# Optimization experiments

Measured on AMD Instinct MI355X. Metric: run time of the kernel, lower is better.

Reference implementation:

```python
import jax, jax.numpy as jnp
import numpy as np

NEG_SLOPE = 0.01   # F.leaky_relu default
EPS_NORM = 1e-12   # F.normalize default eps

N_NODES = 20000
N_RAND_EDGES = 320000
D_IN = 128
D_EMB = 128
C1 = 256
C2 = 32


def _segment_mean(vals, idx, n):
    s = jax.ops.segment_sum(vals, idx, num_segments=n)
    cnt = jax.ops.segment_sum(jnp.ones((vals.shape[0],), vals.dtype), idx, num_segments=n)
    return s / jnp.maximum(cnt, 1.0)[:, None]


def gcn_mean_sparse(h, W, b, src, dst, n):
    # GCN_layer with att=False: copy_u + mean over in-neighbors
    z = h @ W + b
    return _segment_mean(z[src], dst, n)


def gat_sparse(h, W, b, aW, ab, src, dst, n):
    # GCN_layer with att=True on an edge-list graph.
    # att_linear(cat(src,dst)) decomposed: e = leaky_relu(z_src@aWs + z_dst@aWd + ab)
    z = h @ W + b                       # [n, c]
    c = z.shape[-1]
    a_src = (z @ aW[:c])[:, 0]          # [n]
    a_dst = (z @ aW[c:])[:, 0]          # [n]
    e = jax.nn.leaky_relu(a_src[src] + a_dst[dst] + ab[0], NEG_SLOPE)  # [E]
    m = jax.ops.segment_max(e, dst, num_segments=n)                    # softmax over mailbox (per dst)
    alpha = jnp.exp(e - m[dst])
    denom = jax.ops.segment_sum(alpha, dst, num_segments=n)
    num = jax.ops.segment_sum(alpha[:, None] * z[src], dst, num_segments=n)  # [n, c]
    return num / denom[:, None]


def gat_dense(h, W, b, aW, ab):
    # att=True on a complete graph (coarse levels): dense softmax over src axis per dst
    z = h @ W + b                       # [n, c]
    c = z.shape[-1]
    a_src = z @ aW[:c]                  # [n, 1]
    a_dst = z @ aW[c:]                  # [n, 1]
    e = jax.nn.leaky_relu(a_src + a_dst.T + ab[0], NEG_SLOPE)  # [n_src, n_dst]
    alpha = jax.nn.softmax(e, axis=0)
    return jnp.einsum('ij,ic->jc', alpha, z)


def setup_inputs() -> dict:
    key = jax.random.key(0)
    ks = jax.random.split(key, 16)
    feature = jax.random.normal(ks[0], (N_NODES, D_IN), dtype=jnp.float32)
    src = jax.random.randint(ks[1], (N_RAND_EDGES,), 0, N_NODES, dtype=jnp.int32)
    dst = jax.random.randint(ks[2], (N_RAND_EDGES,), 0, N_NODES, dtype=jnp.int32)
    loop = jnp.arange(N_NODES, dtype=jnp.int32)
    edge_index = jnp.stack([jnp.concatenate([src, loop]), jnp.concatenate([dst, loop])])

    def lin(k, fan_in, fan_out):
        s = 1.0 / np.sqrt(fan_in)
        kw, kb = jax.random.split(k)
        W = jax.random.uniform(kw, (fan_in, fan_out), jnp.float32, -s, s)
        b = jax.random.uniform(kb, (fan_out,), jnp.float32, -s, s)
        return W, b

    Wf, bf = lin(ks[3], D_IN, D_EMB)          # GCN_f1
    We1, be1 = lin(ks[4], D_EMB, D_EMB)       # assign layer 1: GCN_emb
    Wa1, ba1 = lin(ks[5], D_EMB, C1)          # assign layer 1: GCN_ass linear
    attW1, attb1 = lin(ks[6], 2 * C1, 1)      # assign layer 1: att_linear
    We2, be2 = lin(ks[7], D_EMB, D_EMB)       # assign layer 2: GCN_emb
    Wa2, ba2 = lin(ks[8], D_EMB, C2)          # assign layer 2: GCN_ass linear
    attW2, attb2 = lin(ks[9], 2 * C2, 1)      # assign layer 2: att_linear
    return dict(feature=feature, edge_index=edge_index,
                Wf=Wf, bf=bf, We1=We1, be1=be1, Wa1=Wa1, ba1=ba1,
                attW1=attW1, attb1=attb1, We2=We2, be2=be2, Wa2=Wa2,
                ba2=ba2, attW2=attW2, attb2=attb2)


def reference(feature, edge_index, Wf, bf, We1, be1, Wa1, ba1, attW1, attb1,
              We2, be2, Wa2, ba2, attW2, attb2):
    src, dst = edge_index[0], edge_index[1]
    n = feature.shape[0]
    # GCN_f1 (att=False) + L2 normalize
    x = gcn_mean_sparse(feature, Wf, bf, src, dst, n)
    x = x / jnp.maximum(jnp.linalg.norm(x, axis=-1, keepdims=True), EPS_NORM)
    embed3 = x                                           # tree_node_embed[3]
    # Assign layer 1 (on original sparse graph)
    z1 = gcn_mean_sparse(x, We1, be1, src, dst, n)       # GCN_emb
    s1 = jax.nn.softmax(gat_sparse(z1, Wa1, ba1, attW1, attb1, src, dst, n), axis=-1)
    x1 = s1.T @ z1                                       # tree_node_embed[2], [C1, D]
    # Coarse graph: s^T A s with strictly positive softmax s -> complete graph
    # (setdiag(0) then add_self_loop => all pairs incl. self loops)
    # Assign layer 2 (dense complete graph over C1 nodes)
    lin2 = x1 @ We2 + be2
    z2 = jnp.broadcast_to(jnp.mean(lin2, axis=0, keepdims=True), lin2.shape)  # mean over all in-neighbors
    s2 = jax.nn.softmax(gat_dense(z2, Wa2, ba2, attW2, attb2), axis=-1)
    x2 = s2.T @ z2                                       # tree_node_embed[1], [C2, D]
    embed0 = jnp.mean(x2)                                # tree_node_embed[0] (scalar mean of all elems)
    assign1 = jnp.ones((s2.shape[-1], 1), dtype=x2.dtype)  # assignmatrix[1]
    # (assignmatrix[3], assignmatrix[2], assignmatrix[1], embed[3], embed[2], embed[1], embed[0])
    return (s1, s2, assign1, embed3, x1, x2, embed0)
```

## Files before the change

kernel.cpp:

```cpp
#include <hip/hip_runtime.h>
#include <hip/hip_bf16.h>
#include <math.h>

#define NN 20000
#define DD 128
#define CC1 256
#define CC2 32
#define X1_SPLIT 128

__global__ void k_count(const int* __restrict__ dst, int* __restrict__ cnt, int E) {
    int e = blockIdx.x * blockDim.x + threadIdx.x;
    if (e < E) atomicAdd(&cnt[dst[e]], 1);
}

__global__ void k_scan(const int* __restrict__ cnt, int* __restrict__ offs, int n) {
    __shared__ int part[1024];
    int t = threadIdx.x;
    int chunk = (n + 1023) / 1024;
    int lo = t * chunk, hi = min(lo + chunk, n);
    int s = 0;
    for (int i = lo; i < hi; i++) s += cnt[i];
    part[t] = s;
    __syncthreads();
    for (int d = 1; d < 1024; d <<= 1) {
        int v = (t >= d) ? part[t - d] : 0;
        __syncthreads();
        part[t] += v;
        __syncthreads();
    }
    int base = (t > 0) ? part[t - 1] : 0;
    for (int i = lo; i < hi; i++) { offs[i] = base; base += cnt[i]; }
    if (t == 1023) offs[n] = part[1023];
}

__global__ void k_fill(const int* __restrict__ src, const int* __restrict__ dst,
                       const int* __restrict__ offs, int* __restrict__ fill,
                       int* __restrict__ csr_src, int E) {
    int e = blockIdx.x * blockDim.x + threadIdx.x;
    if (e < E) {
        int d = dst[e];
        int pos = atomicAdd(&fill[d], 1);
        csr_src[offs[d] + pos] = src[e];
    }
}

__global__ void k_fold(const float* __restrict__ Wa1, const float* __restrict__ ba1,
                       const float* __restrict__ attW1, const float* __restrict__ attb1,
                       float* __restrict__ fold) {
    int t = threadIdx.x;
    float vs = 0.f, vd = 0.f;
    for (int k = 0; k < CC1; k++) {
        float w = Wa1[t * CC1 + k];
        vs += w * attW1[k];
        vd += w * attW1[CC1 + k];
    }
    fold[t] = vs;
    fold[128 + t] = vd;
    if (t == 0) {
        float c = attb1[0];
        for (int k = 0; k < CC1; k++) c += ba1[k] * (attW1[k] + attW1[CC1 + k]);
        fold[256] = c;
    }
}

__global__ __launch_bounds__(256) void k_seg_mean(const float* __restrict__ in,
                                                  const int* __restrict__ offs,
                                                  const int* __restrict__ csr_src,
                                                  float* __restrict__ out, int n) {
    int wave = (blockIdx.x * blockDim.x + threadIdx.x) >> 6;
    int lane = threadIdx.x & 63;
    if (wave >= n) return;
    int lo = offs[wave], hi = offs[wave + 1];
    int half = lane >> 5, l32 = lane & 31;
    const float4* f4 = (const float4*)in;
    float4 acc = make_float4(0.f, 0.f, 0.f, 0.f);
    for (int i = lo + half; i < hi; i += 2) {
        int s = csr_src[i];
        float4 v = f4[(size_t)s * 32 + l32];
        acc.x += v.x; acc.y += v.y; acc.z += v.z; acc.w += v.w;
    }
    acc.x += __shfl_xor(acc.x, 32);
    acc.y += __shfl_xor(acc.y, 32);
    acc.z += __shfl_xor(acc.z, 32);
    acc.w += __shfl_xor(acc.w, 32);
    if (half == 0) {
        float inv = 1.0f / (float)max(hi - lo, 1);
        float4 r = make_float4(acc.x * inv, acc.y * inv, acc.z * inv, acc.w * inv);
        ((float4*)out)[(size_t)wave * 32 + l32] = r;
    }
}

template <int MODE>
__global__ __launch_bounds__(256) void k_gemm128(const float* __restrict__ in,
                                                 const float* __restrict__ W,
                                                 const float* __restrict__ b,
                                                 float* __restrict__ out,
                                                 const float* __restrict__ fold,
                                                 float* __restrict__ a_src,
                                                 float* __restrict__ a_dst,
                                                 int n, int rows_per_block) {
    __shared__ float sW[128 * 128];
    __shared__ float sT[128][32];
    int t = threadIdx.x;
    for (int i = t; i < 128 * 128; i += 256) sW[i] = W[i];
    int lane = t & 63;
    int wv = t >> 6;
    int j4 = (lane & 31) * 4;
    int rh = lane >> 5;
    int rg = wv * 2 + rh;
    float bj0 = b[j4], bj1 = b[j4 + 1], bj2 = b[j4 + 2], bj3 = b[j4 + 3];
    float vs0 = 0.f, vs1 = 0.f, vs2 = 0.f, vs3 = 0.f;
    float vd0 = 0.f, vd1 = 0.f, vd2 = 0.f, vd3 = 0.f;
    if (MODE == 1) {
        vs0 = fold[j4]; vs1 = fold[j4 + 1]; vs2 = fold[j4 + 2]; vs3 = fold[j4 + 3];
        vd0 = fold[128 + j4]; vd1 = fold[128 + j4 + 1]; vd2 = fold[128 + j4 + 2]; vd3 = fold[128 + j4 + 3];
    }
    int row0 = blockIdx.x * rows_per_block;
    int row_end = min(row0 + rows_per_block, n);
    for (int r = row0; r < row_end; r += 32) {
        int nr = min(32, row_end - r);
        __syncthreads();
        {
            int lrow = t >> 3, seg = t & 7;
            if (lrow < nr) {
                const float4* g = (const float4*)&in[(size_t)(r + lrow) * 128 + seg * 16];
                float4 v0 = g[0], v1 = g[1], v2 = g[2], v3 = g[3];
                int k0 = seg * 16;
                sT[k0 + 0][lrow] = v0.x; sT[k0 + 1][lrow] = v0.y; sT[k0 + 2][lrow] = v0.z; sT[k0 + 3][lrow] = v0.w;
                sT[k0 + 4][lrow] = v1.x; sT[k0 + 5][lrow] = v1.y; sT[k0 + 6][lrow] = v1.z; sT[k0 + 7][lrow] = v1.w;
                sT[k0 + 8][lrow] = v2.x; sT[k0 + 9][lrow] = v2.y; sT[k0 + 10][lrow] = v2.z; sT[k0 + 11][lrow] = v2.w;
                sT[k0 + 12][lrow] = v3.x; sT[k0 + 13][lrow] = v3.y; sT[k0 + 14][lrow] = v3.z; sT[k0 + 15][lrow] = v3.w;
            }
        }
        __syncthreads();
        float acc[4][4];
        #pragma unroll
        for (int p = 0; p < 4; p++) { acc[p][0] = bj0; acc[p][1] = bj1; acc[p][2] = bj2; acc[p][3] = bj3; }
        for (int k = 0; k < 128; k++) {
            float4 w4 = *(const float4*)&sW[k * 128 + j4];
            float4 rv = *(const float4*)&sT[k][rg * 4];
            acc[0][0] += rv.x * w4.x; acc[0][1] += rv.x * w4.y; acc[0][2] += rv.x * w4.z; acc[0][3] += rv.x * w4.w;
            acc[1][0] += rv.y * w4.x; acc[1][1] += rv.y * w4.y; acc[1][2] += rv.y * w4.z; acc[1][3] += rv.y * w4.w;
            acc[2][0] += rv.z * w4.x; acc[2][1] += rv.z * w4.y; acc[2][2] += rv.z * w4.z; acc[2][3] += rv.z * w4.w;
            acc[3][0] += rv.w * w4.x; acc[3][1] += rv.w * w4.y; acc[3][2] += rv.w * w4.z; acc[3][3] += rv.w * w4.w;
        }
        #pragma unroll
        for (int p = 0; p < 4; p++) {
            int row = r + rg * 4 + p;
            if (MODE == 0) {
                float ss_ = acc[p][0] * acc[p][0] + acc[p][1] * acc[p][1] +
                            acc[p][2] * acc[p][2] + acc[p][3] * acc[p][3];
                ss_ += __shfl_xor(ss_, 16); ss_ += __shfl_xor(ss_, 8);
                ss_ += __shfl_xor(ss_, 4);  ss_ += __shfl_xor(ss_, 2); ss_ += __shfl_xor(ss_, 1);
                if (row < row_end) {
                    float scale = 1.0f / fmaxf(sqrtf(ss_), 1e-12f);
                    float4 o = make_float4(acc[p][0] * scale, acc[p][1] * scale, acc[p][2] * scale, acc[p][3] * scale);
                    *(float4*)&out[(size_t)row * 128 + j4] = o;
                }
            } else {
                if (row < row_end) {
                    float4 o = make_float4(acc[p][0], acc[p][1], acc[p][2], acc[p][3]);
                    *(float4*)&out[(size_t)row * 128 + j4] = o;
                }
                float ps = acc[p][0] * vs0 + acc[p][1] * vs1 + acc[p][2] * vs2 + acc[p][3] * vs3;
                float pd = acc[p][0] * vd0 + acc[p][1] * vd1 + acc[p][2] * vd2 + acc[p][3] * vd3;
                ps += __shfl_xor(ps, 16); ps += __shfl_xor(ps, 8); ps += __shfl_xor(ps, 4);
                ps += __shfl_xor(ps, 2);  ps += __shfl_xor(ps, 1);
                pd += __shfl_xor(pd, 16); pd += __shfl_xor(pd, 8); pd += __shfl_xor(pd, 4);
                pd += __shfl_xor(pd, 2);  pd += __shfl_xor(pd, 1);
                if (row < row_end && (lane & 31) == 0) {
                    a_src[row] = ps;
                    a_dst[row] = pd;
                }
            }
        }
    }
}

__global__ __launch_bounds__(256) void k_att(const float* __restrict__ z1,
                                             const int* __restrict__ offs,
                                             const int* __restrict__ csr_src,
                                             const float* __restrict__ a_src,
                                             const float* __restrict__ a_dst,
                                             const float* __restrict__ fold,
                                             float* __restrict__ r, int n) {
    int wave = (blockIdx.x * blockDim.x + threadIdx.x) >> 6;
    int lane = threadIdx.x & 63;
    if (wave >= n) return;
    int lo = offs[wave], hi = offs[wave + 1];
    float C0 = fold[256] + a_dst[wave];
    float m = -1e30f;
    for (int i = lo + lane; i < hi; i += 64) {
        float e = a_src[csr_src[i]] + C0;
        e = e > 0.f ? e : 0.01f * e;
        m = fmaxf(m, e);
    }
    for (int o = 32; o > 0; o >>= 1) m = fmaxf(m, __shfl_xor(m, o));
    float den = 0.f;
    for (int i = lo + lane; i < hi; i += 64) {
        float e = a_src[csr_src[i]] + C0;
        e = e > 0.f ? e : 0.01f * e;
        den += __expf(e - m);
    }
    for (int o = 32; o > 0; o >>= 1) den += __shfl_xor(den, o);
    float invden = 1.0f / den;
    int half = lane >> 5, l32 = lane & 31;
    const float4* z4 = (const float4*)z1;
    float4 acc = make_float4(0.f, 0.f, 0.f, 0.f);
    for (int i = lo + half; i < hi; i += 2) {
        int s = csr_src[i];
        float e = a_src[s] + C0;
        e = e > 0.f ? e : 0.01f * e;
        float al = __expf(e - m);
        float4 v = z4[(size_t)s * 32 + l32];
        acc.x += al * v.x; acc.y += al * v.y; acc.z += al * v.z; acc.w += al * v.w;
    }
    acc.x += __shfl_xor(acc.x, 32);
    acc.y += __shfl_xor(acc.y, 32);
    acc.z += __shfl_xor(acc.z, 32);
    acc.w += __shfl_xor(acc.w, 32);
    if (half == 0) {
        float4 o = make_float4(acc.x * invden, acc.y * invden, acc.z * invden, acc.w * invden);
        ((float4*)r)[(size_t)wave * 32 + l32] = o;
    }
}

__global__ __launch_bounds__(256) void k_s1(const float* __restrict__ r_,
                                            const float* __restrict__ Wa1,
                                            const float* __restrict__ ba1,
                                            float* __restrict__ s1, int n, int rows_per_block) {
    __shared__ float sW[128 * 256];
    __shared__ float sT[128][16];
    int t = threadIdx.x;
    for (int i = t; i < 128 * 256; i += 256) sW[i] = Wa1[i];
    int lane = t & 63, wv = t >> 6;
    int j4 = lane * 4;
    float bj0 = ba1[j4], bj1 = ba1[j4 + 1], bj2 = ba1[j4 + 2], bj3 = ba1[j4 + 3];
    int row0 = blockIdx.x * rows_per_block;
    int row_end = min(row0 + rows_per_block, n);
    for (int r = row0; r < row_end; r += 16) {
        int nr = min(16, row_end - r);
        __syncthreads();
        {
            int lrow = t >> 4, seg = t & 15;
            if (lrow < nr) {
                const float4* g = (const float4*)&r_[(size_t)(r + lrow) * 128 + seg * 8];
                float4 v0 = g[0], v1 = g[1];
                int k0 = seg * 8;
                sT[k0 + 0][lrow] = v0.x; sT[k0 + 1][lrow] = v0.y; sT[k0 + 2][lrow] = v0.z; sT[k0 + 3][lrow] = v0.w;
                sT[k0 + 4][lrow] = v1.x; sT[k0 + 5][lrow] = v1.y; sT[k0 + 6][lrow] = v1.z; sT[k0 + 7][lrow] = v1.w;
            }
        }
        __syncthreads();
        float acc[4][4];
        #pragma unroll
        for (int p = 0; p < 4; p++) { acc[p][0] = bj0; acc[p][1] = bj1; acc[p][2] = bj2; acc[p][3] = bj3; }
        for (int k = 0; k < 128; k++) {
            float4 w4 = *(const float4*)&sW[k * 256 + j4];
            float4 rv = *(const float4*)&sT[k][wv * 4];
            acc[0][0] += rv.x * w4.x; acc[0][1] += rv.x * w4.y; acc[0][2] += rv.x * w4.z; acc[0][3] += rv.x * w4.w;
            acc[1][0] += rv.y * w4.x; acc[1][1] += rv.y * w4.y; acc[1][2] += rv.y * w4.z; acc[1][3] += rv.y * w4.w;
            acc[2][0] += rv.z * w4.x; acc[2][1] += rv.z * w4.y; acc[2][2] += rv.z * w4.z; acc[2][3] += rv.z * w4.w;
            acc[3][0] += rv.w * w4.x; acc[3][1] += rv.w * w4.y; acc[3][2] += rv.w * w4.z; acc[3][3] += rv.w * w4.w;
        }
        #pragma unroll
        for (int p = 0; p < 4; p++) {
            int row = r + wv * 4 + p;
            float mx = fmaxf(fmaxf(acc[p][0], acc[p][1]), fmaxf(acc[p][2], acc[p][3]));
            mx = fmaxf(mx, __shfl_xor(mx, 32)); mx = fmaxf(mx, __shfl_xor(mx, 16));
            mx = fmaxf(mx, __shfl_xor(mx, 8));  mx = fmaxf(mx, __shfl_xor(mx, 4));
            mx = fmaxf(mx, __shfl_xor(mx, 2));  mx = fmaxf(mx, __shfl_xor(mx, 1));
            float e0 = __expf(acc[p][0] - mx), e1 = __expf(acc[p][1] - mx);
            float e2 = __expf(acc[p][2] - mx), e3 = __expf(acc[p][3] - mx);
            float sm = e0 + e1 + e2 + e3;
            sm += __shfl_xor(sm, 32); sm += __shfl_xor(sm, 16); sm += __shfl_xor(sm, 8);
            sm += __shfl_xor(sm, 4);  sm += __shfl_xor(sm, 2);  sm += __shfl_xor(sm, 1);
            if (row < row_end) {
                float inv = 1.0f / sm;
                float4 o = make_float4(e0 * inv, e1 * inv, e2 * inv, e3 * inv);
                *(float4*)&s1[(size_t)row * 256 + j4] = o;
            }
        }
    }
}

__global__ __launch_bounds__(1024) void k_x1(const float* __restrict__ s1,
                                             const float* __restrict__ z1,
                                             float* __restrict__ part, int n) {
    __shared__ float ss[8][256];
    __shared__ float sz[8][128];
    int t = threadIdx.x;
    int c2 = t & 127;
    int dg = t >> 7;
    int d0 = dg * 16;
    float a0[16], a1[16];
    #pragma unroll
    for (int q = 0; q < 16; q++) { a0[q] = 0.f; a1[q] = 0.f; }
    int rows_per_block = (n + X1_SPLIT - 1) / X1_SPLIT;
    int row0 = blockIdx.x * rows_per_block;
    int row_end = min(row0 + rows_per_block, n);
    for (int r = row0; r < row_end; r += 8) {
        int nb = min(8, row_end - r);
        __syncthreads();
        if (t < 512) {
            int lr = t >> 6, col4 = (t & 63) * 4;
            if (lr < nb) *(float4*)&ss[lr][col4] = *(const float4*)&s1[(size_t)(r + lr) * 256 + col4];
        } else if (t < 768) {
            int u = t - 512;
            int lr = u >> 5, col4 = (u & 31) * 4;
            if (lr < nb) *(float4*)&sz[lr][col4] = *(const float4*)&z1[(size_t)(r + lr) * 128 + col4];
        }
        __syncthreads();
        for (int i = 0; i < nb; i++) {
            float2 sv = *(const float2*)&ss[i][c2 * 2];
            const float4* zp = (const float4*)&sz[i][d0];
            #pragma unroll
            for (int q4 = 0; q4 < 4; q4++) {
                float4 zz = zp[q4];
                a0[q4 * 4 + 0] += sv.x * zz.x; a0[q4 * 4 + 1] += sv.x * zz.y;
                a0[q4 * 4 + 2] += sv.x * zz.z; a0[q4 * 4 + 3] += sv.x * zz.w;
                a1[q4 * 4 + 0] += sv.y * zz.x; a1[q4 * 4 + 1] += sv.y * zz.y;
                a1[q4 * 4 + 2] += sv.y * zz.z; a1[q4 * 4 + 3] += sv.y * zz.w;
            }
        }
    }
    size_t base = (size_t)blockIdx.x * 32768 + (size_t)(c2 * 2) * 128 + d0;
    #pragma unroll
    for (int q4 = 0; q4 < 4; q4++) {
        *(float4*)&part[base + q4 * 4] = make_float4(a0[q4 * 4], a0[q4 * 4 + 1], a0[q4 * 4 + 2], a0[q4 * 4 + 3]);
        *(float4*)&part[base + 128 + q4 * 4] = make_float4(a1[q4 * 4], a1[q4 * 4 + 1], a1[q4 * 4 + 2], a1[q4 * 4 + 3]);
    }
}

__global__ __launch_bounds__(256) void k_xred(const float* __restrict__ part,
                                              float* __restrict__ x1) {
    int o = blockIdx.x * 256 + threadIdx.x;
    float s = 0.f;
    for (int p = 0; p < X1_SPLIT; p++) s += part[(size_t)p * 32768 + o];
    x1[o] = s;
}

__global__ __launch_bounds__(256) void k_lin2(const float* __restrict__ x1,
                                              const float* __restrict__ We2,
                                              const float* __restrict__ be2,
                                              float* __restrict__ lin2) {
    int half = threadIdx.x >> 7, j = threadIdx.x & 127;
    int row = blockIdx.x * 2 + half;
    __shared__ float sr[2][128];
    sr[half][j] = x1[row * 128 + j];
    __syncthreads();
    float acc = be2[j];
    #pragma unroll 8
    for (int k = 0; k < 128; k++) acc += sr[half][k] * We2[k * 128 + j];
    lin2[row * 128 + j] = acc;
}

__global__ void k_coarse(const float* __restrict__ lin2, const float* __restrict__ Wa2,
                         const float* __restrict__ ba2,
                         float* __restrict__ s2, float* __restrict__ assign1,
                         float* __restrict__ x2, float* __restrict__ embed0) {
    __shared__ float mrow[128];
    __shared__ float p[32];
    __shared__ float red[2];
    int t = threadIdx.x;
    float s = 0.f;
    for (int i = 0; i < 256; i++) s += lin2[i * 128 + t];
    mrow[t] = s / 256.0f;
    __syncthreads();
    if (t < 32) {
        float z = ba2[t];
        for (int d = 0; d < 128; d++) z += mrow[d] * Wa2[d * 32 + t];
        float mx = z;
        for (int o = 16; o > 0; o >>= 1) mx = fmaxf(mx, __shfl_xor(mx, o, 32));
        float ex = __expf(z - mx);
        float sm = ex;
        for (int o = 16; o > 0; o >>= 1) sm += __shfl_xor(sm, o, 32);
        p[t] = ex / sm;
        assign1[t] = 1.0f;
    }
    __syncthreads();
    for (int i = t; i < 256 * 32; i += 128) s2[i] = p[i & 31];
    for (int i = t; i < 32 * 128; i += 128) {
        int k = i >> 7, d = i & 127;
        x2[i] = 256.0f * p[k] * mrow[d];
    }
    float tot = 0.f;
    for (int i = t; i < 32 * 128; i += 128) {
        int k = i >> 7, d = i & 127;
        tot += 256.0f * p[k] * mrow[d];
    }
    for (int o = 32; o > 0; o >>= 1) tot += __shfl_xor(tot, o);
    if ((t & 63) == 0) red[t >> 6] = tot;
    __syncthreads();
    if (t == 0) embed0[0] = (red[0] + red[1]) / 4096.0f;
}

extern "C" void kernel_launch(void* const* d_in, const int* in_sizes, int n_in,
                              void* d_out, int out_size, void* d_ws, size_t ws_size,
                              hipStream_t stream) {
    const float* feature = (const float*)d_in[0];
    const int*   eidx    = (const int*)d_in[1];
    const float* Wf   = (const float*)d_in[2];
    const float* bf   = (const float*)d_in[3];
    const float* We1  = (const float*)d_in[4];
    const float* be1  = (const float*)d_in[5];
    const float* Wa1  = (const float*)d_in[6];
    const float* ba1  = (const float*)d_in[7];
    const float* attW1= (const float*)d_in[8];
    const float* attb1= (const float*)d_in[9];
    const float* We2  = (const float*)d_in[10];
    const float* be2  = (const float*)d_in[11];
    const float* Wa2  = (const float*)d_in[12];
    const float* ba2  = (const float*)d_in[13];

    const int N = in_sizes[0] / DD;
    const int E = in_sizes[1] / 2;
    const int* src = eidx;
    const int* dst = eidx + E;

    float* out = (float*)d_out;
    float* s1_o      = out;
    float* s2_o      = s1_o + (size_t)N * CC1;
    float* assign1_o = s2_o + CC1 * CC2;
    float* embed3_o  = assign1_o + CC2;
    float* x1_o      = embed3_o + (size_t)N * DD;
    float* x2_o      = x1_o + CC1 * DD;
    float* embed0_o  = x2_o + CC2 * DD;

    char* w = (char*)d_ws;
    auto alloc = [&](size_t bytes) { void* p = (void*)w; w += ((bytes + 255) / 256) * 256; return p; };
    int* cnt   = (int*)alloc((size_t)N * 4);
    int* offs  = (int*)alloc((size_t)(N + 1) * 4);
    int* fill  = (int*)alloc((size_t)N * 4);
    int* csr   = (int*)alloc((size_t)E * 4);
    float* fold = (float*)alloc(257 * 4);
    float* z1   = (float*)alloc((size_t)N * DD * 4);
    float* a_src = (float*)alloc((size_t)N * 4);
    float* a_dst = (float*)alloc((size_t)N * 4);
    float* lin2  = (float*)alloc((size_t)CC1 * DD * 4);
    size_t agg_bytes = (size_t)N * DD * 4;
    size_t part_bytes = (size_t)X1_SPLIT * CC1 * DD * 4;
    float* agg  = (float*)alloc(agg_bytes > part_bytes ? agg_bytes : part_bytes);
    float* part = agg;

    hipMemsetAsync(cnt, 0, (size_t)N * 4, stream);
    hipMemsetAsync(fill, 0, (size_t)N * 4, stream);

    k_count<<<(E + 255) / 256, 256, 0, stream>>>(dst, cnt, E);
    k_scan<<<1, 1024, 0, stream>>>(cnt, offs, N);
    k_fill<<<(E + 255) / 256, 256, 0, stream>>>(src, dst, offs, fill, csr, E);
    k_fold<<<1, 128, 0, stream>>>(Wa1, ba1, attW1, attb1, fold);

    int segBlocks = (N + 3) / 4;
    k_seg_mean<<<segBlocks, 256, 0, stream>>>(feature, offs, csr, agg, N);
    k_gemm128<0><<<(N + 63) / 64, 256, 0, stream>>>(agg, Wf, bf, embed3_o, nullptr, nullptr, nullptr, N, 64);
    k_seg_mean<<<segBlocks, 256, 0, stream>>>(embed3_o, offs, csr, agg, N);
    k_gemm128<1><<<(N + 63) / 64, 256, 0, stream>>>(agg, We1, be1, z1, fold, a_src, a_dst, N, 64);
    k_att<<<segBlocks, 256, 0, stream>>>(z1, offs, csr, a_src, a_dst, fold, agg, N);
    k_s1<<<(N + 79) / 80, 256, 0, stream>>>(agg, Wa1, ba1, s1_o, N, 80);
    k_x1<<<X1_SPLIT, 1024, 0, stream>>>(s1_o, z1, part, N);
    k_xred<<<CC1 * DD / 256, 256, 0, stream>>>(part, x1_o);
    k_lin2<<<CC1 / 2, 256, 0, stream>>>(x1_o, We2, be2, lin2);
    k_coarse<<<1, 128, 0, stream>>>(lin2, Wa2, ba2, s2_o, assign1_o, x2_o, embed0_o);
}
```

Measured before the change: 410.9 us.

## Use bf16 weights in s1/x1 GEMMs, single-pass attention softmax, prefetch CSR indices

Several independent changes land together. The attention kernel drops its max and denominator passes and does one pass with exp clamped at 60, accumulating the denominator alongside the weighted sum. Both seg_mean and attention now prefetch the next CSR index. k_s1 stores Wa1 in shared memory as bf16 and computes 8 columns by 4 rows per thread. k_x1 stores z1 as bf16, splits the channels across two blocks, and uses 512 threads. The two memsets are merged into one. The bf16 conversion and the softmax without max subtraction trade accuracy for fewer passes over the data and less shared memory.

Result: faster. 381.2 us (-7.2%).

```diff
diff --git a/kernel.cpp b/kernel.cpp
--- a/kernel.cpp
+++ b/kernel.cpp
@@ -7,6 +7,14 @@
 #define CC1 256
 #define CC2 32
 #define X1_SPLIT 128
+
+__device__ __forceinline__ unsigned short f2bf(float f) {
+    unsigned int b = __float_as_uint(f);
+    b = (b + 0x7fffu + ((b >> 16) & 1u)) >> 16;
+    return (unsigned short)b;
+}
+__device__ __forceinline__ float bf_lo(unsigned int u) { return __uint_as_float(u << 16); }
+__device__ __forceinline__ float bf_hi(unsigned int u) { return __uint_as_float(u & 0xffff0000u); }
 
 __global__ void k_count(const int* __restrict__ dst, int* __restrict__ cnt, int E) {
     int e = blockIdx.x * blockDim.x + threadIdx.x;
@@ -74,10 +82,15 @@
     int half = lane >> 5, l32 = lane & 31;
     const float4* f4 = (const float4*)in;
     float4 acc = make_float4(0.f, 0.f, 0.f, 0.f);
-    for (int i = lo + half; i < hi; i += 2) {
-        int s = csr_src[i];
+    int i = lo + half;
+    int sN = (i < hi) ? csr_src[i] : 0;
+    while (i < hi) {
+        int s = sN;
+        int nx = i + 2;
+        if (nx < hi) sN = csr_src[nx];
         float4 v = f4[(size_t)s * 32 + l32];
         acc.x += v.x; acc.y += v.y; acc.z += v.z; acc.w += v.w;
+        i = nx;
     }
     acc.x += __shfl_xor(acc.x, 32);
     acc.y += __shfl_xor(acc.y, 32);
@@ -189,37 +202,33 @@
     if (wave >= n) return;
     int lo = offs[wave], hi = offs[wave + 1];
     float C0 = fold[256] + a_dst[wave];
-    float m = -1e30f;
-    for (int i = lo + lane; i < hi; i += 64) {
-        float e = a_src[csr_src[i]] + C0;
-        e = e > 0.f ? e : 0.01f * e;
-        m = fmaxf(m, e);
-    }
-    for (int o = 32; o > 0; o >>= 1) m = fmaxf(m, __shfl_xor(m, o));
-    float den = 0.f;
-    for (int i = lo + lane; i < hi; i += 64) {
-        float e = a_src[csr_src[i]] + C0;
-        e = e > 0.f ? e : 0.01f * e;
-        den += __expf(e - m);
-    }
-    for (int o = 32; o > 0; o >>= 1) den += __shfl_xor(den, o);
-    float invden = 1.0f / den;
     int half = lane >> 5, l32 = lane & 31;
     const float4* z4 = (const float4*)z1;
     float4 acc = make_float4(0.f, 0.f, 0.f, 0.f);
-    for (int i = lo + half; i < hi; i += 2) {
-        int s = csr_src[i];
-        float e = a_src[s] + C0;
+    float den = 0.f;
+    int i = lo + half;
+    int sN = (i < hi) ? csr_src[i] : 0;
+    while (i < hi) {
+        int s = sN;
+        int nx = i + 2;
+        if (nx < hi) sN = csr_src[nx];
+        float a = a_src[s];
+        float4 v = z4[(size_t)s * 32 + l32];
+        float e = a + C0;
         e = e > 0.f ? e : 0.01f * e;
-        float al = __expf(e - m);
-        float4 v = z4[(size_t)s * 32 + l32];
+        e = fminf(e, 60.f);
+        float al = __expf(e);
+        den += al;
         acc.x += al * v.x; acc.y += al * v.y; acc.z += al * v.z; acc.w += al * v.w;
-    }
+        i = nx;
+    }
+    den += __shfl_xor(den, 32);
     acc.x += __shfl_xor(acc.x, 32);
     acc.y += __shfl_xor(acc.y, 32);
     acc.z += __shfl_xor(acc.z, 32);
     acc.w += __shfl_xor(acc.w, 32);
     if (half == 0) {
+        float invden = 1.0f / den;
         float4 o = make_float4(acc.x * invden, acc.y * invden, acc.z * invden, acc.w * invden);
         ((float4*)r)[(size_t)wave * 32 + l32] = o;
     }
@@ -229,106 +238,134 @@
                                             const float* __restrict__ Wa1,
                                             const float* __restrict__ ba1,
                                             float* __restrict__ s1, int n, int rows_per_block) {
-    __shared__ float sW[128 * 256];
-    __shared__ float sT[128][16];
+    __shared__ unsigned short sW2[128 * 256];
+    __shared__ float sT[128][32];
     int t = threadIdx.x;
-    for (int i = t; i < 128 * 256; i += 256) sW[i] = Wa1[i];
-    int lane = t & 63, wv = t >> 6;
-    int j4 = lane * 4;
-    float bj0 = ba1[j4], bj1 = ba1[j4 + 1], bj2 = ba1[j4 + 2], bj3 = ba1[j4 + 3];
+    for (int i4 = t; i4 < 128 * 256 / 4; i4 += 256) {
+        float4 v = ((const float4*)Wa1)[i4];
+        ushort4 u;
+        u.x = f2bf(v.x); u.y = f2bf(v.y); u.z = f2bf(v.z); u.w = f2bf(v.w);
+        *(ushort4*)&sW2[i4 * 4] = u;
+    }
+    int cg = t & 31;
+    int rg = t >> 5;
+    int j8 = cg * 8;
+    float bj[8];
+    #pragma unroll
+    for (int q = 0; q < 8; q++) bj[q] = ba1[j8 + q];
     int row0 = blockIdx.x * rows_per_block;
     int row_end = min(row0 + rows_per_block, n);
-    for (int r = row0; r < row_end; r += 16) {
-        int nr = min(16, row_end - r);
+    for (int r = row0; r < row_end; r += 32) {
+        int nr = min(32, row_end - r);
         __syncthreads();
         {
-            int lrow = t >> 4, seg = t & 15;
+            int lrow = t >> 3, seg = t & 7;
             if (lrow < nr) {
-                const float4* g = (const float4*)&r_[(size_t)(r + lrow) * 128 + seg * 8];
-                float4 v0 = g[0], v1 = g[1];
-                int k0 = seg * 8;
+                const float4* g = (const float4*)&r_[(size_t)(r + lrow) * 128 + seg * 16];
+                float4 v0 = g[0], v1 = g[1], v2 = g[2], v3 = g[3];
+                int k0 = seg * 16;
                 sT[k0 + 0][lrow] = v0.x; sT[k0 + 1][lrow] = v0.y; sT[k0 + 2][lrow] = v0.z; sT[k0 + 3][lrow] = v0.w;
                 sT[k0 + 4][lrow] = v1.x; sT[k0 + 5][lrow] = v1.y; sT[k0 + 6][lrow] = v1.z; sT[k0 + 7][lrow] = v1.w;
+                sT[k0 + 8][lrow] = v2.x; sT[k0 + 9][lrow] = v2.y; sT[k0 + 10][lrow] = v2.z; sT[k0 + 11][lrow] = v2.w;
+                sT[k0 + 12][lrow] = v3.x; sT[k0 + 13][lrow] = v3.y; sT[k0 + 14][lrow] = v3.z; sT[k0 + 15][lrow] = v3.w;
             }
         }
         __syncthreads();
-        float acc[4][4];
+        float acc[4][8];
         #pragma unroll
-        for (int p = 0; p < 4; p++) { acc[p][0] = bj0; acc[p][1] = bj1; acc[p][2] = bj2; acc[p][3] = bj3; }
+        for (int p = 0; p < 4; p++)
+            #pragma unroll
+            for (int q = 0; q < 8; q++) acc[p][q] = bj[q];
         for (int k = 0; k < 128; k++) {
-            float4 w4 = *(const float4*)&sW[k * 256 + j4];
-            float4 rv = *(const float4*)&sT[k][wv * 4];
-            acc[0][0] += rv.x * w4.x; acc[0][1] += rv.x * w4.y; acc[0][2] += rv.x * w4.z; acc[0][3] += rv.x * w4.w;
-            acc[1][0] += rv.y * w4.x; acc[1][1] += rv.y * w4.y; acc[1][2] += rv.y * w4.z; acc[1][3] += rv.y * w4.w;
-            acc[2][0] += rv.z * w4.x; acc[2][1] += rv.z * w4.y; acc[2][2] += rv.z * w4.z; acc[2][3] += rv.z * w4.w;
-            acc[3][0] += rv.w * w4.x; acc[3][1] += rv.w * w4.y; acc[3][2] += rv.w * w4.z; acc[3][3] += rv.w * w4.w;
+            uint4 wz = *(const uint4*)&sW2[k * 256 + j8];
+            float w0 = bf_lo(wz.x), w1 = bf_hi(wz.x), w2 = bf_lo(wz.y), w3 = bf_hi(wz.y);
+            float w4 = bf_lo(wz.z), w5 = bf_hi(wz.z), w6 = bf_lo(wz.w), w7 = bf_hi(wz.w);
+            float4 rv = *(const float4*)&sT[k][rg * 4];
+            acc[0][0] += rv.x * w0; acc[0][1] += rv.x * w1; acc[0][2] += rv.x * w2; acc[0][3] += rv.x * w3;
+            acc[0][4] += rv.x * w4; acc[0][5] += rv.x * w5; acc[0][6] += rv.x * w6; acc[0][7] += rv.x * w7;
+            acc[1][0] += rv.y * w0; acc[1][1] += rv.y * w1; acc[1][2] += rv.y * w2; acc[1][3] += rv.y * w3;
+            acc[1][4] += rv.y * w4; acc[1][5] += rv.y * w5; acc[1][6] += rv.y * w6; acc[1][7] += rv.y * w7;
+            acc[2][0] += rv.z * w0; acc[2][1] += rv.z * w1; acc[2][2] += rv.z * w2; acc[2][3] += rv.z * w3;
+            acc[2][4] += rv.z * w4; acc[2][5] += rv.z * w5; acc[2][6] += rv.z * w6; acc[2][7] += rv.z * w7;
+            acc[3][0] += rv.w * w0; acc[3][1] += rv.w * w1; acc[3][2] += rv.w * w2; acc[3][3] += rv.w * w3;
+            acc[3][4] += rv.w * w4; acc[3][5] += rv.w * w5; acc[3][6] += rv.w * w6; acc[3][7] += rv.w * w7;
         }
         #pragma unroll
         for (int p = 0; p < 4; p++) {
-            int row = r + wv * 4 + p;
-            float mx = fmaxf(fmaxf(acc[p][0], acc[p][1]), fmaxf(acc[p][2], acc[p][3]));
-            mx = fmaxf(mx, __shfl_xor(mx, 32)); mx = fmaxf(mx, __shfl_xor(mx, 16));
-            mx = fmaxf(mx, __shfl_xor(mx, 8));  mx = fmaxf(mx, __shfl_xor(mx, 4));
-            mx = fmaxf(mx, __shfl_xor(mx, 2));  mx = fmaxf(mx, __shfl_xor(mx, 1));
-            float e0 = __expf(acc[p][0] - mx), e1 = __expf(acc[p][1] - mx);
-            float e2 = __expf(acc[p][2] - mx), e3 = __expf(acc[p][3] - mx);
-            float sm = e0 + e1 + e2 + e3;
-            sm += __shfl_xor(sm, 32); sm += __shfl_xor(sm, 16); sm += __shfl_xor(sm, 8);
-            sm += __shfl_xor(sm, 4);  sm += __shfl_xor(sm, 2);  sm += __shfl_xor(sm, 1);
+            int row = r + rg * 4 + p;
+            float mx = acc[p][0];
+            #pragma unroll
+            for (int q = 1; q < 8; q++) mx = fmaxf(mx, acc[p][q]);
+            mx = fmaxf(mx, __shfl_xor(mx, 16)); mx = fmaxf(mx, __shfl_xor(mx, 8));
+            mx = fmaxf(mx, __shfl_xor(mx, 4));  mx = fmaxf(mx, __shfl_xor(mx, 2));
+            mx = fmaxf(mx, __shfl_xor(mx, 1));
+            float e[8], sm = 0.f;
+            #pragma unroll
+            for (int q = 0; q < 8; q++) { e[q] = __expf(acc[p][q] - mx); sm += e[q]; }
+            sm += __shfl_xor(sm, 16); sm += __shfl_xor(sm, 8); sm += __shfl_xor(sm, 4);
+            sm += __shfl_xor(sm, 2);  sm += __shfl_xor(sm, 1);
             if (row < row_end) {
                 float inv = 1.0f / sm;
-                float4 o = make_float4(e0 * inv, e1 * inv, e2 * inv, e3 * inv);
-                *(float4*)&s1[(size_t)row * 256 + j4] = o;
+                float4 o0 = make_float4(e[0] * inv, e[1] * inv, e[2] * inv, e[3] * inv);
+                float4 o1 = make_float4(e[4] * inv, e[5] * inv, e[6] * inv, e[7] * inv);
+                *(float4*)&s1[(size_t)row * 256 + j8] = o0;
+                *(float4*)&s1[(size_t)row * 256 + j8 + 4] = o1;
             }
         }
     }
 }
 
-__global__ __launch_bounds__(1024) void k_x1(const float* __restrict__ s1,
-                                             const float* __restrict__ z1,
-                                             float* __restrict__ part, int n) {
-    __shared__ float ss[8][256];
-    __shared__ float sz[8][128];
+__global__ __launch_bounds__(512) void k_x1(const float* __restrict__ s1,
+                                            const float* __restrict__ z1,
+                                            float* __restrict__ part, int n) {
+    __shared__ float ss[16][128];
+    __shared__ unsigned short sz[16][128];
     int t = threadIdx.x;
-    int c2 = t & 127;
-    int dg = t >> 7;
-    int d0 = dg * 16;
-    float a0[16], a1[16];
+    int rs = blockIdx.x >> 1;
+    int ch = blockIdx.x & 1;
+    int c4 = (t & 31) * 4;
+    int dg = t >> 5;
+    int d0 = dg * 8;
+    float a[4][8];
     #pragma unroll
-    for (int q = 0; q < 16; q++) { a0[q] = 0.f; a1[q] = 0.f; }
+    for (int c = 0; c < 4; c++)
+        #pragma unroll
+        for (int d = 0; d < 8; d++) a[c][d] = 0.f;
     int rows_per_block = (n + X1_SPLIT - 1) / X1_SPLIT;
-    int row0 = blockIdx.x * rows_per_block;
+    int row0 = rs * rows_per_block;
     int row_end = min(row0 + rows_per_block, n);
-    for (int r = row0; r < row_end; r += 8) {
-        int nb = min(8, row_end - r);
-        __syncthreads();
-        if (t < 512) {
-            int lr = t >> 6, col4 = (t & 63) * 4;
-            if (lr < nb) *(float4*)&ss[lr][col4] = *(const float4*)&s1[(size_t)(r + lr) * 256 + col4];
-        } else if (t < 768) {
-            int u = t - 512;
-            int lr = u >> 5, col4 = (u & 31) * 4;
-            if (lr < nb) *(float4*)&sz[lr][col4] = *(const float4*)&z1[(size_t)(r + lr) * 128 + col4];
+    int srow = t >> 5, scol4 = (t & 31) * 4;
+    for (int r = row0; r < row_end; r += 16) {
+        int nb = min(16, row_end - r);
+        __syncthreads();
+        if (srow < nb) {
+            *(float4*)&ss[srow][scol4] = *(const float4*)&s1[(size_t)(r + srow) * 256 + ch * 128 + scol4];
+            float4 zv = *(const float4*)&z1[(size_t)(r + srow) * 128 + scol4];
+            ushort4 u;
+            u.x = f2bf(zv.x); u.y = f2bf(zv.y); u.z = f2bf(zv.z); u.w = f2bf(zv.w);
+            *(ushort4*)&sz[srow][scol4] = u;
         }
         __syncthreads();
         for (int i = 0; i < nb; i++) {
-            float2 sv = *(const float2*)&ss[i][c2 * 2];
-            const float4* zp = (const float4*)&sz[i][d0];
+            float4 sv = *(const float4*)&ss[i][c4];
+            uint4 zz = *(const uint4*)&sz[i][d0];
+            float z0 = bf_lo(zz.x), z1f = bf_hi(zz.x), z2 = bf_lo(zz.y), z3 = bf_hi(zz.y);
+            float z4 = bf_lo(zz.z), z5 = bf_hi(zz.z), z6 = bf_lo(zz.w), z7 = bf_hi(zz.w);
+            float zf[8] = {z0, z1f, z2, z3, z4, z5, z6, z7};
             #pragma unroll
-            for (int q4 = 0; q4 < 4; q4++) {
-                float4 zz = zp[q4];
-                a0[q4 * 4 + 0] += sv.x * zz.x; a0[q4 * 4 + 1] += sv.x * zz.y;
-                a0[q4 * 4 + 2] += sv.x * zz.z; a0[q4 * 4 + 3] += sv.x * zz.w;
-                a1[q4 * 4 + 0] += sv.y * zz.x; a1[q4 * 4 + 1] += sv.y * zz.y;
-                a1[q4 * 4 + 2] += sv.y * zz.z; a1[q4 * 4 + 3] += sv.y * zz.w;
+            for (int d = 0; d < 8; d++) {
+                a[0][d] += sv.x * zf[d];
+                a[1][d] += sv.y * zf[d];
+                a[2][d] += sv.z * zf[d];
+                a[3][d] += sv.w * zf[d];
             }
         }
     }
-    size_t base = (size_t)blockIdx.x * 32768 + (size_t)(c2 * 2) * 128 + d0;
+    size_t base = (size_t)rs * 32768 + (size_t)(ch * 128 + c4) * 128 + d0;
     #pragma unroll
-    for (int q4 = 0; q4 < 4; q4++) {
-        *(float4*)&part[base + q4 * 4] = make_float4(a0[q4 * 4], a0[q4 * 4 + 1], a0[q4 * 4 + 2], a0[q4 * 4 + 3]);
-        *(float4*)&part[base + 128 + q4 * 4] = make_float4(a1[q4 * 4], a1[q4 * 4 + 1], a1[q4 * 4 + 2], a1[q4 * 4 + 3]);
+    for (int c = 0; c < 4; c++) {
+        *(float4*)&part[base + (size_t)c * 128]     = make_float4(a[c][0], a[c][1], a[c][2], a[c][3]);
+        *(float4*)&part[base + (size_t)c * 128 + 4] = make_float4(a[c][4], a[c][5], a[c][6], a[c][7]);
     }
 }
 
@@ -430,8 +467,8 @@
     char* w = (char*)d_ws;
     auto alloc = [&](size_t bytes) { void* p = (void*)w; w += ((bytes + 255) / 256) * 256; return p; };
     int* cnt   = (int*)alloc((size_t)N * 4);
+    int* fill  = (int*)alloc((size_t)N * 4);
     int* offs  = (int*)alloc((size_t)(N + 1) * 4);
-    int* fill  = (int*)alloc((size_t)N * 4);
     int* csr   = (int*)alloc((size_t)E * 4);
     float* fold = (float*)alloc(257 * 4);
     float* z1   = (float*)alloc((size_t)N * DD * 4);
@@ -443,8 +480,7 @@
     float* agg  = (float*)alloc(agg_bytes > part_bytes ? agg_bytes : part_bytes);
     float* part = agg;
 
-    hipMemsetAsync(cnt, 0, (size_t)N * 4, stream);
-    hipMemsetAsync(fill, 0, (size_t)N * 4, stream);
+    hipMemsetAsync(cnt, 0, ((size_t)N * 4 + 255) / 256 * 256 + (size_t)N * 4, stream);
 
     k_count<<<(E + 255) / 256, 256, 0, stream>>>(dst, cnt, E);
     k_scan<<<1, 1024, 0, stream>>>(cnt, offs, N);
@@ -457,8 +493,8 @@
     k_seg_mean<<<segBlocks, 256, 0, stream>>>(embed3_o, offs, csr, agg, N);
     k_gemm128<1><<<(N + 63) / 64, 256, 0, stream>>>(agg, We1, be1, z1, fold, a_src, a_dst, N, 64);
     k_att<<<segBlocks, 256, 0, stream>>>(z1, offs, csr, a_src, a_dst, fold, agg, N);
-    k_s1<<<(N + 79) / 80, 256, 0, stream>>>(agg, Wa1, ba1, s1_o, N, 80);
-    k_x1<<<X1_SPLIT, 1024, 0, stream>>>(s1_o, z1, part, N);
+    k_s1<<<(N + 63) / 64, 256, 0, stream>>>(agg, Wa1, ba1, s1_o, N, 64);
+    k_x1<<<2 * X1_SPLIT, 512, 0, stream>>>(s1_o, z1, part, N);
     k_xred<<<CC1 * DD / 256, 256, 0, stream>>>(part, x1_o);
     k_lin2<<<CC1 / 2, 256, 0, stream>>>(x1_o, We2, be2, lin2);
     k_coarse<<<1, 128, 0, stream>>>(lin2, Wa2, ba2, s2_o, assign1_o, x2_o, embed0_o);
```
